# Performance work log

Measured on AMD Instinct MI355X. Metric: run time of the kernel, lower is better.

Reference implementation:

```python
import jax, jax.numpy as jnp
import numpy as np
from jax import lax

GROUPS = 4
KH = KW = 3
K = KH * KW
STRIDE = (1, 1)
PAD = ((1, 1), (1, 1))
DIL = (1, 1)


def _bilinear_gather(padded, py, px):
    # padded: (B,C,Hp,Wp); py,px: (B,C,K,Ho,Wo) float sample positions in padded coords
    B, C, Hp, Wp = padded.shape
    bi = jnp.arange(B)[:, None, None, None, None]
    ci = jnp.arange(C)[None, :, None, None, None]
    y0 = jnp.floor(py)
    x0 = jnp.floor(px)
    wy = py - y0
    wx = px - x0
    out = jnp.zeros(py.shape, padded.dtype)
    corners = ((0, 0, (1 - wy) * (1 - wx)), (0, 1, (1 - wy) * wx),
               (1, 0, wy * (1 - wx)), (1, 1, wy * wx))
    for dy, dx, w in corners:
        yy = y0 + dy
        xx = x0 + dx
        valid = (yy >= 0) & (yy < Hp) & (xx >= 0) & (xx < Wp)  # zero outside (implicit zero padding)
        yc = jnp.clip(yy, 0, Hp - 1).astype(jnp.int32)
        xc = jnp.clip(xx, 0, Wp - 1).astype(jnp.int32)
        out = out + jnp.where(valid, padded[bi, ci, yc, xc] * w, 0.0)
    return out


def deform_conv2d(inps, weight, bias, weight_off, bias_off):
    B, C, H, W = inps.shape
    # offset/mask predicting conv (grouped, same geometry as the main conv)
    off = lax.conv_general_dilated(inps, weight_off, STRIDE, PAD, rhs_dilation=DIL,
                                   feature_group_count=GROUPS,
                                   dimension_numbers=('NCHW', 'OIHW', 'NCHW'))
    off = off + bias_off[None, :, None, None]
    Ho, Wo = off.shape[2], off.shape[3]
    off = off.reshape(B, 3, C * K, Ho, Wo)  # (B, dim+1, C*K, Ho, Wo)
    dy = off[:, 0].reshape(B, C, K, Ho, Wo)
    dx = off[:, 1].reshape(B, C, K, Ho, Wo)
    # softmax across the GROUP axis, as in the original reshape(b,1,groups,-1,h,w).softmax(dim=2)
    mask = jax.nn.softmax(off[:, 2].reshape(B, GROUPS, (C // GROUPS) * K, Ho, Wo), axis=1)
    mask = mask.reshape(B, C, K, Ho, Wo)

    padded = jnp.pad(inps, ((0, 0), (0, 0), PAD[0], PAD[1]))
    ky, kx = jnp.meshgrid(jnp.arange(KH), jnp.arange(KW), indexing='ij')
    ky = ky.ravel().astype(inps.dtype)
    kx = kx.ravel().astype(inps.dtype)
    oh = jnp.arange(Ho, dtype=inps.dtype)
    ow = jnp.arange(Wo, dtype=inps.dtype)
    # sample position per (batch, in-channel, kernel tap, output pixel)
    py = oh[None, None, None, :, None] * STRIDE[0] + ky[None, None, :, None, None] * DIL[0] + dy
    px = ow[None, None, None, None, :] * STRIDE[1] + kx[None, None, :, None, None] * DIL[1] + dx

    sampled = _bilinear_gather(padded, py, px) * mask  # (B,C,K,Ho,Wo)

    Cout = weight.shape[0]
    Cg = C // GROUPS
    wg = weight.reshape(GROUPS, Cout // GROUPS, Cg, K)          # (g, o, c, k)
    sg = sampled.reshape(B, GROUPS, Cg, K, Ho, Wo)              # (b, g, c, k, h, w)
    out = jnp.einsum('bgckhw,gock->bgohw', sg, wg).reshape(B, Cout, Ho, Wo)
    return out + bias[None, :, None, None]


def setup_inputs() -> dict:
    key = jax.random.key(0)
    k0, k1, k2, k3 = jax.random.split(key, 4)
    B, C, H, W = 8, 64, 64, 64
    Cout = 64
    inps = jax.random.normal(k0, (B, C, H, W), dtype=jnp.float32)
    weight = jax.random.normal(k1, (Cout, C // GROUPS, KH, KW), dtype=jnp.float32) * 0.05
    bias = jax.random.normal(k2, (Cout,), dtype=jnp.float32) * 0.05
    # small offset-conv weights -> offsets of a few pixels, non-saturated softmax
    weight_off = jax.random.normal(k3, (C * K * 3, C // GROUPS, KH, KW), dtype=jnp.float32) * 0.05
    bias_off = jnp.zeros((C * K * 3,), dtype=jnp.float32)
    return {'inps': inps, 'weight': weight, 'bias': bias,
            'weight_off': weight_off, 'bias_off': bias_off}


def reference(inps, weight, bias, weight_off, bias_off):
    return deform_conv2d(inps, weight, bias, weight_off, bias_off)
```

## Files before the change

kernel.cpp:

```cpp
#include <hip/hip_runtime.h>

typedef __attribute__((ext_vector_type(8))) short short8;
typedef __attribute__((ext_vector_type(4))) float f32x4;

__device__ __forceinline__ unsigned short bf16rne(float f) {
    unsigned u = __float_as_uint(f);
    u += 0x7FFFu + ((u >> 16) & 1u);
    return (unsigned short)(u >> 16);
}
__device__ __forceinline__ float bf16dec(unsigned short h) {
    return __uint_as_float((unsigned)h << 16);
}
__device__ __forceinline__ unsigned cvtpk2(float lo, float hi) {
    unsigned r;
    asm("v_cvt_pk_bf16_f32 %0, %1, %2" : "=v"(r) : "v"(lo), "v"(hi));
    return r;
}

extern __shared__ char smem[];


#define IMC4_OFF   0
#define PATCH4_OFF 37376
#define SX4_OFF    62720
#define LGX4_OFF   72960
#define LDS_V4     77312
#define OTB4_OFF   37376

#define PWOFF_U32  138240
#define PWM_U32    5120
#define WS_NEEDED  ((size_t)(PWOFF_U32 + PWM_U32) * 4)

__global__ __launch_bounds__(256)
void pack_weights(const float* __restrict__ wmain,
                  const float* __restrict__ woff,
                  unsigned* __restrict__ pw)
{
    int idx = blockIdx.x * 256 + threadIdx.x;
    if (idx < PWOFF_U32) {
        int j2   = idx & 3;
        int lane = (idx >> 2) & 63;
        int rest = idx >> 8;
        int kt   = rest % 5;
        int t    = rest / 5;
        int comp = t / 36, r36 = t - comp * 36;
        int jw   = r36 / 9, ntg = r36 - jw * 9;
        int ochb = comp * 576 + jw * 144 + ntg * 16;
        int g    = ochb / 432;
        int ktf  = (9 * g) >> 1;
        int och  = ochb + (lane & 15);
        int ck   = (ktf + kt) * 32 + (lane >> 4) * 8 + j2 * 2 - g * 144;
        float v0 = 0.f, v1 = 0.f;
        if ((unsigned)ck < 144u)       v0 = woff[(size_t)och * 144 + ck];
        if ((unsigned)(ck + 1) < 144u) v1 = woff[(size_t)och * 144 + ck + 1];
        pw[idx] = (unsigned)bf16rne(v0) | ((unsigned)bf16rne(v1) << 16);
    } else if (idx < PWOFF_U32 + PWM_U32) {
        int m    = idx - PWOFF_U32;
        int j2   = m & 3;
        int lane = (m >> 2) & 63;
        int rest = m >> 8;
        int jw   = rest / 5, pair = rest - jw * 5;
        int och  = jw * 16 + (lane & 15);
        int w0   = pair * 32 + (lane >> 4) * 8 + j2 * 2;
        float v0 = (w0 < 144)     ? wmain[(size_t)och * 144 + w0]     : 0.f;
        float v1 = (w0 + 1 < 144) ? wmain[(size_t)och * 144 + w0 + 1] : 0.f;
        pw[idx] = (unsigned)bf16rne(v0) | ((unsigned)bf16rne(v1) << 16);
    }
}

__global__ __launch_bounds__(256, 2)
void deform_v4(const float* __restrict__ inps,
               const float* __restrict__ bmain,
               const float* __restrict__ boff,
               const unsigned short* __restrict__ pwoff,
               const unsigned short* __restrict__ pwm,
               float* __restrict__ out)
{
    unsigned short* IMC   = (unsigned short*)(smem + IMC4_OFF);
    unsigned short* PATCH = (unsigned short*)(smem + PATCH4_OFF);
    unsigned short* SX    = (unsigned short*)(smem + SX4_OFF);
    unsigned short* LGX   = (unsigned short*)(smem + LGX4_OFF);
    float*          OTB   = (float*)(smem + OTB4_OFF);

    const int tid  = threadIdx.x;
    const int lane = tid & 63;
    const int jw   = __builtin_amdgcn_readfirstlane(tid >> 6);
    const int slot = lane & 15;
    const int q    = lane >> 4;

    const int b    = blockIdx.x >> 7;
    const int tile = blockIdx.x & 127;
    const int ty0  = (tile >> 3) << 2;
    const int tx0  = (tile & 7) << 3;

    const float* inb = inps + (size_t)b * 262144;

    for (int e = tid; e < 12288; e += 256) {
        int c = e / 192, rem = e - c * 192;
        int y = rem >> 4, x = rem & 15;
        int gy = ty0 + y - 4, gx = tx0 + x - 4;
        float v = 0.f;
        if ((unsigned)gy < 64u && (unsigned)gx < 64u)
            v = inb[(c * 64 + gy) * 64 + gx];
        PATCH[c * 198 + rem] = bf16rne(v);
    }
    __syncthreads();

    {
        const int px  = tid >> 3;
        const int sub = tid & 7;
        const int pyr = px >> 3, pxx = px & 7;
        unsigned* dst = (unsigned*)(IMC + px * 584);
        #pragma unroll 4
        for (int i = 0; i < 36; ++i) {
            int kk = i * 16 + sub * 2;
            int c0 = kk / 9,        r0 = kk - c0 * 9;
            int c1 = (kk + 1) / 9,  r1 = (kk + 1) - c1 * 9;
            unsigned short a  = PATCH[c0 * 198 + (pyr + r0 / 3 + 3) * 16 + pxx + r0 % 3 + 3];
            unsigned short bb = PATCH[c1 * 198 + (pyr + r1 / 3 + 3) * 16 + pxx + r1 % 3 + 3];
            dst[(unsigned)kk >> 1] = (unsigned)a | ((unsigned)bb << 16);
        }
    }
    __syncthreads();

    f32x4 aco[2] = {{0.f,0.f,0.f,0.f},{0.f,0.f,0.f,0.f}};

    auto pair_mfma = [&](int pair) {
        const short8 bfr = ((const short8*)pwm)[(jw * 5 + pair) * 64 + lane];
        #pragma unroll
        for (int mt = 0; mt < 2; ++mt) {
            const short8 a8 = *(const short8*)(SX + jw * 1280 + (mt * 16 + slot) * 40 + q * 8);
            aco[mt] = __builtin_amdgcn_mfma_f32_16x16x32_bf16(a8, bfr, aco[mt], 0, 0, 0);
        }
    };

    for (int ntg = 0; ntg < 9; ++ntg) {
        f32x4 aD[2] = {{0.f,0.f,0.f,0.f},{0.f,0.f,0.f,0.f}};
        f32x4 aX[2] = {{0.f,0.f,0.f,0.f},{0.f,0.f,0.f,0.f}};
        f32x4 aM[2] = {{0.f,0.f,0.f,0.f},{0.f,0.f,0.f,0.f}};

        auto gemm3 = [&](f32x4* acc, int comp) {
            const int ochb = comp * 576 + jw * 144 + ntg * 16;
            const int g    = ochb / 432;
            const int ktf  = (9 * g) >> 1;
            const int t    = comp * 36 + jw * 9 + ntg;
            const short8* wp  = (const short8*)pwoff + t * 320 + lane;
            const short8* ap0 = (const short8*)(smem + IMC4_OFF);
            #pragma unroll
            for (int kt = 0; kt < 5; ++kt) {
                const short8 bfr = wp[kt * 64];
                const int ktg = ktf + kt;
                #pragma unroll
                for (int mt = 0; mt < 2; ++mt) {
                    const short8 af = ap0[(mt * 16 + slot) * 73 + ktg * 4 + q];
                    acc[mt] = __builtin_amdgcn_mfma_f32_16x16x32_bf16(af, bfr, acc[mt], 0, 0, 0);
                }
            }
            const float bo = boff[ochb + slot];
            #pragma unroll
            for (int mt = 0; mt < 2; ++mt) {
                acc[mt][0] += bo; acc[mt][1] += bo; acc[mt][2] += bo; acc[mt][3] += bo;
            }
        };
        gemm3(aD, 0); gemm3(aX, 1); gemm3(aM, 2);

        #pragma unroll
        for (int mt = 0; mt < 2; ++mt)
        #pragma unroll
        for (int r = 0; r < 4; ++r) {
            int pxr = mt * 16 + q * 4 + r;
            LGX[pxr * 68 + slot * 4 + jw] = bf16rne(aM[mt][r]);
        }
        __syncthreads();

        const int rr  = ntg * 16 + slot;
        const int cg  = rr / 9;
        const int kk9 = rr - cg * 9;
        const int kyk = kk9 / 3, kxk = kk9 - kyk * 3;
        const int c   = jw * 16 + cg;
        const float* inc = inb + c * 4096;
        const int pbase = c * 198;
        const int par = ntg & 1;

        #pragma unroll
        for (int mt = 0; mt < 2; ++mt)
        #pragma unroll
        for (int r = 0; r < 4; ++r) {
            const int pxr = mt * 16 + q * 4 + r;
            const int pyr = pxr >> 3, pxx = pxr & 7;
            const float own = aM[mt][r];

            const uint2 lg = *(const uint2*)(LGX + pxr * 68 + slot * 4);
            float s4 = __expf(bf16dec((unsigned short)(lg.x & 0xFFFF)) - own)
                     + __expf(bf16dec((unsigned short)(lg.x >> 16))    - own)
                     + __expf(bf16dec((unsigned short)(lg.y & 0xFFFF)) - own)
                     + __expf(bf16dec((unsigned short)(lg.y >> 16))    - own);
            const float msk = 1.0f / s4;

            float pyf = (float)(ty0 + pyr + kyk - 1) + aD[mt][r];
            float pxf = (float)(tx0 + pxx + kxk - 1) + aX[mt][r];
            float y0f = floorf(pyf), x0f = floorf(pxf);
            float wy = pyf - y0f, wx = pxf - x0f;
            int iy0 = (int)y0f, ix0 = (int)x0f;
            float w00 = (1.f - wy) * (1.f - wx), w01 = (1.f - wy) * wx;
            float w10 = wy * (1.f - wx),         w11 = wy * wx;

            int ly0 = iy0 - ty0 + 4;
            int lx0 = ix0 - tx0 + 4;
            float v;
            if ((unsigned)ly0 < 11u && (unsigned)lx0 < 15u) {
                const int a = pbase + ly0 * 16 + lx0;
                v = w00 * bf16dec(PATCH[a])      + w01 * bf16dec(PATCH[a + 1])
                  + w10 * bf16dec(PATCH[a + 16]) + w11 * bf16dec(PATCH[a + 17]);
            } else {
                v = 0.f;
                if ((unsigned)iy0 < 64u) {
                    if ((unsigned)ix0 < 64u)       v += w00 * inc[iy0 * 64 + ix0];
                    if ((unsigned)(ix0 + 1) < 64u) v += w01 * inc[iy0 * 64 + ix0 + 1];
                }
                if ((unsigned)(iy0 + 1) < 64u) {
                    if ((unsigned)ix0 < 64u)       v += w10 * inc[(iy0 + 1) * 64 + ix0];
                    if ((unsigned)(ix0 + 1) < 64u) v += w11 * inc[(iy0 + 1) * 64 + ix0 + 1];
                }
            }
            SX[jw * 1280 + pxr * 40 + par * 16 + slot] = bf16rne(v * msk);
        }

        if (ntg & 1)  { asm volatile("" ::: "memory"); pair_mfma(ntg >> 1); }
        if (ntg == 8) { asm volatile("" ::: "memory"); pair_mfma(4); }
        __syncthreads();
    }

    {
        const int o = jw * 16 + slot;
        const float bo = bmain[o];
        #pragma unroll
        for (int mt = 0; mt < 2; ++mt)
        #pragma unroll
        for (int r = 0; r < 4; ++r)
            OTB[o * 33 + mt * 16 + q * 4 + r] = aco[mt][r] + bo;
    }
    __syncthreads();
    #pragma unroll
    for (int i = 0; i < 8; ++i) {
        int f  = i * 256 + tid;
        int oo = f >> 5, pp = f & 31;
        out[(size_t)(b * 64 + oo) * 4096 + (ty0 + (pp >> 3)) * 64 + (tx0 + (pp & 7))] =
            OTB[oo * 33 + pp];
    }
}

#define V2IMC_OFF   0
#define V2S_OFF     37376
#define V2LGX_OFF   74752
#define V2LDS_BYTES 78848

__global__ __launch_bounds__(256, 2)
void deform_v2(const float* __restrict__ inps,
               const float* __restrict__ wmain,
               const float* __restrict__ bmain,
               const float* __restrict__ woff,
               const float* __restrict__ boff,
               float* __restrict__ out)
{
    unsigned short* IMC  = (unsigned short*)(smem + V2IMC_OFF);
    unsigned short* SBUF = (unsigned short*)(smem + V2S_OFF);
    unsigned short* LGX  = (unsigned short*)(smem + V2LGX_OFF);
    float* PATCH = (float*)(smem + V2S_OFF);
    float* OTB   = (float*)(smem + V2IMC_OFF);

    const int tid  = threadIdx.x;
    const int lane = tid & 63;
    const int jw   = __builtin_amdgcn_readfirstlane(tid >> 6);
    const int slot = lane & 15;
    const int q    = lane >> 4;

    const int b    = blockIdx.x >> 7;
    const int tile = blockIdx.x & 127;
    const int ty0  = (tile >> 3) << 2;
    const int tx0  = (tile & 7) << 3;

    const float* inb = inps + (size_t)b * 262144;

    for (int e = tid; e < 64 * 60; e += 256) {
        int ch = e / 60, rem = e - ch * 60;
        int iy = rem / 10, ix = rem - iy * 10;
        int gy = ty0 + iy - 1, gx = tx0 + ix - 1;
        float v = 0.f;
        if ((unsigned)gy < 64u && (unsigned)gx < 64u)
            v = inb[(ch * 64 + gy) * 64 + gx];
        PATCH[ch * 61 + rem] = v;
    }
    __syncthreads();
    {
        const int px  = tid >> 3;
        const int sub = tid & 7;
        const int pyr = px >> 3, pxx = px & 7;
        unsigned short* dst = IMC + px * 584;
        for (int i = 0; i < 36; ++i) {
            int kk = sub * 72 + 2 * i;
            float v0, v1;
            { int c = kk / 9, r9 = kk - c * 9, ky = r9 / 3, kx = r9 - ky * 3;
              v0 = PATCH[c * 61 + (pyr + ky) * 10 + (pxx + kx)]; }
            { int k1 = kk + 1; int c = k1 / 9, r9 = k1 - c * 9, ky = r9 / 3, kx = r9 - ky * 3;
              v1 = PATCH[c * 61 + (pyr + ky) * 10 + (pxx + kx)]; }
            *(unsigned*)(dst + kk) = cvtpk2(v0, v1);
        }
    }
    __syncthreads();

    for (int ntg = 0; ntg < 9; ++ntg) {
        f32x4 aD[2] = {{0.f,0.f,0.f,0.f},{0.f,0.f,0.f,0.f}};
        f32x4 aX[2] = {{0.f,0.f,0.f,0.f},{0.f,0.f,0.f,0.f}};
        f32x4 aM[2] = {{0.f,0.f,0.f,0.f},{0.f,0.f,0.f,0.f}};

        auto gemm3 = [&](f32x4* acc, int comp) {
            const int ochb = comp * 576 + jw * 144 + ntg * 16;
            const int g    = ochb / 432;
            const int ktf  = (9 * g) >> 1;
            const int ch0  = g * 18;
            const int och  = ochb + slot;
            #pragma unroll
            for (int kt = 0; kt < 5; ++kt) {
                const int ktg   = ktf + kt;
                const int chunk = ktg * 4 + q;
                short8 bfr;
                if ((unsigned)(chunk - ch0) < 18u) {
                    const float4* wp = (const float4*)(woff + (size_t)och * 144 + (chunk - ch0) * 8);
                    float4 w0 = wp[0], w1 = wp[1];
                    union { unsigned u[4]; short8 s; } cv;
                    cv.u[0] = cvtpk2(w0.x, w0.y); cv.u[1] = cvtpk2(w0.z, w0.w);
                    cv.u[2] = cvtpk2(w1.x, w1.y); cv.u[3] = cvtpk2(w1.z, w1.w);
                    bfr = cv.s;
                } else {
                    bfr = short8{0,0,0,0,0,0,0,0};
                }
                #pragma unroll
                for (int mt = 0; mt < 2; ++mt) {
                    const short8* ap = (const short8*)(smem + V2IMC_OFF +
                                        (mt * 16 + slot) * 1168 + ktg * 64 + q * 16);
                    acc[mt] = __builtin_amdgcn_mfma_f32_16x16x32_bf16(*ap, bfr, acc[mt], 0, 0, 0);
                }
            }
            const float bo = boff[ochb + slot];
            #pragma unroll
            for (int mt = 0; mt < 2; ++mt) {
                acc[mt][0] += bo; acc[mt][1] += bo; acc[mt][2] += bo; acc[mt][3] += bo;
            }
        };
        gemm3(aD, 0); gemm3(aX, 1); gemm3(aM, 2);

        #pragma unroll
        for (int mt = 0; mt < 2; ++mt)
        #pragma unroll
        for (int r = 0; r < 4; ++r) {
            int pxr = mt * 16 + q * 4 + r;
            LGX[(jw * 32 + pxr) * 16 + slot] = bf16rne(aM[mt][r]);
        }
        __syncthreads();

        const int rr  = ntg * 16 + slot;
        const int cg  = rr / 9;
        const int kk9 = rr - cg * 9;
        const int kyk = kk9 / 3, kxk = kk9 - kyk * 3;
        const float* inc = inb + (jw * 16 + cg) * 4096;

        #pragma unroll
        for (int mt = 0; mt < 2; ++mt)
        #pragma unroll
        for (int r = 0; r < 4; ++r) {
            const int pxr = mt * 16 + q * 4 + r;
            const int pyr = pxr >> 3, pxx = pxr & 7;
            float own = aM[mt][r];
            float l0 = (jw == 0) ? own : bf16dec(LGX[(0 * 32 + pxr) * 16 + slot]);
            float l1 = (jw == 1) ? own : bf16dec(LGX[(1 * 32 + pxr) * 16 + slot]);
            float l2 = (jw == 2) ? own : bf16dec(LGX[(2 * 32 + pxr) * 16 + slot]);
            float l3 = (jw == 3) ? own : bf16dec(LGX[(3 * 32 + pxr) * 16 + slot]);
            float m4 = fmaxf(fmaxf(l0, l1), fmaxf(l2, l3));
            float s4 = __expf(l0 - m4) + __expf(l1 - m4) + __expf(l2 - m4) + __expf(l3 - m4);
            float msk = __expf(own - m4) / s4;

            float pyf = (float)(ty0 + pyr + kyk - 1) + aD[mt][r];
            float pxf = (float)(tx0 + pxx + kxk - 1) + aX[mt][r];
            float y0f = floorf(pyf), x0f = floorf(pxf);
            float wy = pyf - y0f, wx = pxf - x0f;
            int iy0 = (int)y0f, ix0 = (int)x0f;
            float w00 = (1.f - wy) * (1.f - wx), w01 = (1.f - wy) * wx;
            float w10 = wy * (1.f - wx),         w11 = wy * wx;
            float v = 0.f;
            if ((unsigned)iy0 < 64u) {
                if ((unsigned)ix0 < 64u)       v += w00 * inc[iy0 * 64 + ix0];
                if ((unsigned)(ix0 + 1) < 64u) v += w01 * inc[iy0 * 64 + ix0 + 1];
            }
            if ((unsigned)(iy0 + 1) < 64u) {
                if ((unsigned)ix0 < 64u)       v += w10 * inc[(iy0 + 1) * 64 + ix0];
                if ((unsigned)(ix0 + 1) < 64u) v += w11 * inc[(iy0 + 1) * 64 + ix0 + 1];
            }
            SBUF[pxr * 584 + jw * 144 + rr] = bf16rne(v * msk);
        }
        __syncthreads();
    }

    {
        f32x4 aco2[2] = {{0.f,0.f,0.f,0.f},{0.f,0.f,0.f,0.f}};
        const int ktf = (9 * jw) >> 1;
        const int ch0 = jw * 18;
        const int o   = jw * 16 + slot;
        #pragma unroll
        for (int kt = 0; kt < 5; ++kt) {
            const int ktg   = ktf + kt;
            const int chunk = ktg * 4 + q;
            short8 bfr;
            if ((unsigned)(chunk - ch0) < 18u) {
                const float4* wp = (const float4*)(wmain + (size_t)o * 144 + (chunk - ch0) * 8);
                float4 w0 = wp[0], w1 = wp[1];
                union { unsigned u[4]; short8 s; } cv;
                cv.u[0] = cvtpk2(w0.x, w0.y); cv.u[1] = cvtpk2(w0.z, w0.w);
                cv.u[2] = cvtpk2(w1.x, w1.y); cv.u[3] = cvtpk2(w1.z, w1.w);
                bfr = cv.s;
            } else {
                bfr = short8{0,0,0,0,0,0,0,0};
            }
            #pragma unroll
            for (int mt = 0; mt < 2; ++mt) {
                const short8* ap = (const short8*)(smem + V2S_OFF +
                                    (mt * 16 + slot) * 1168 + ktg * 64 + q * 16);
                aco2[mt] = __builtin_amdgcn_mfma_f32_16x16x32_bf16(*ap, bfr, aco2[mt], 0, 0, 0);
            }
        }
        const float bo = bmain[o];
        __syncthreads();
        #pragma unroll
        for (int mt = 0; mt < 2; ++mt)
        #pragma unroll
        for (int r = 0; r < 4; ++r)
            OTB[o * 33 + mt * 16 + q * 4 + r] = aco2[mt][r] + bo;
    }
    __syncthreads();
    #pragma unroll
    for (int i = 0; i < 8; ++i) {
        int f  = i * 256 + tid;
        int oo = f >> 5, pp = f & 31;
        out[(size_t)(b * 64 + oo) * 4096 + (ty0 + (pp >> 3)) * 64 + (tx0 + (pp & 7))] =
            OTB[oo * 33 + pp];
    }
}

extern "C" void kernel_launch(void* const* d_in, const int* in_sizes, int n_in,
                              void* d_out, int out_size, void* d_ws, size_t ws_size,
                              hipStream_t stream) {
    const float* inps   = (const float*)d_in[0];
    const float* weight = (const float*)d_in[1];
    const float* bias   = (const float*)d_in[2];
    const float* woff   = (const float*)d_in[3];
    const float* boff   = (const float*)d_in[4];
    float* outp = (float*)d_out;

    if (ws_size >= WS_NEEDED) {
        unsigned* pw = (unsigned*)d_ws;
        pack_weights<<<dim3(560), dim3(256), 0, stream>>>(weight, woff, pw);
        hipFuncSetAttribute((const void*)deform_v4,
                            hipFuncAttributeMaxDynamicSharedMemorySize, LDS_V4);
        deform_v4<<<dim3(1024), dim3(256), LDS_V4, stream>>>(
            inps, bias, boff,
            (const unsigned short*)pw,
            (const unsigned short*)(pw + PWOFF_U32), outp);
    } else {
        hipFuncSetAttribute((const void*)deform_v2,
                            hipFuncAttributeMaxDynamicSharedMemorySize, V2LDS_BYTES);
        deform_v2<<<dim3(1024), dim3(256), V2LDS_BYTES, stream>>>(
            inps, weight, bias, woff, boff, outp);
    }
}
```

Before: 141.9 us.

## Drop explicit im2col buffer; read offset-conv A operands from channel-minor patch

Removes the explicit im2col staging pass and its large LDS buffer. The input patch is now stored channel-minor (pixel-major, padded stride 66), so the offset-conv MFMA A fragments are read straight from the patch. The offset weights are repacked so K runs tap-major with channels contiguous. This frees LDS, letting launch bounds rise from 2 to 4 blocks per CU for more occupancy, at the cost of scattered, possibly bank-conflicting patch reads during bilinear sampling and changed SX/LGX strides.

```diff
diff --git a/kernel.cpp b/kernel.cpp
--- a/kernel.cpp
+++ b/kernel.cpp
@@ -20,12 +20,11 @@
 extern __shared__ char smem[];
 
 
-#define IMC4_OFF   0
-#define PATCH4_OFF 37376
-#define SX4_OFF    62720
-#define LGX4_OFF   72960
-#define LDS_V4     77312
-#define OTB4_OFF   37376
+#define PT5_OFF   0
+#define SX5_OFF   25344
+#define LGX5_OFF  34560
+#define LDS_V5    38656
+#define OTB5_OFF  0
 
 #define PWOFF_U32  138240
 #define PWM_U32    5120
@@ -49,10 +48,13 @@
         int g    = ochb / 432;
         int ktf  = (9 * g) >> 1;
         int och  = ochb + (lane & 15);
-        int ck   = (ktf + kt) * 32 + (lane >> 4) * 8 + j2 * 2 - g * 144;
+        int w    = (ktf + kt) * 32 + (lane >> 4) * 8 + j2 * 2 - g * 144;
         float v0 = 0.f, v1 = 0.f;
-        if ((unsigned)ck < 144u)       v0 = woff[(size_t)och * 144 + ck];
-        if ((unsigned)(ck + 1) < 144u) v1 = woff[(size_t)och * 144 + ck + 1];
+        if ((unsigned)w < 144u)
+            v0 = woff[(size_t)och * 144 + (w & 15) * 9 + (w >> 4)];
+        int w1 = w + 1;
+        if ((unsigned)w1 < 144u)
+            v1 = woff[(size_t)och * 144 + (w1 & 15) * 9 + (w1 >> 4)];
         pw[idx] = (unsigned)bf16rne(v0) | ((unsigned)bf16rne(v1) << 16);
     } else if (idx < PWOFF_U32 + PWM_U32) {
         int m    = idx - PWOFF_U32;
@@ -68,25 +70,26 @@
     }
 }
 
-__global__ __launch_bounds__(256, 2)
-void deform_v4(const float* __restrict__ inps,
+__global__ __launch_bounds__(256, 4)
+void deform_v5(const float* __restrict__ inps,
                const float* __restrict__ bmain,
                const float* __restrict__ boff,
                const unsigned short* __restrict__ pwoff,
                const unsigned short* __restrict__ pwm,
                float* __restrict__ out)
 {
-    unsigned short* IMC   = (unsigned short*)(smem + IMC4_OFF);
-    unsigned short* PATCH = (unsigned short*)(smem + PATCH4_OFF);
-    unsigned short* SX    = (unsigned short*)(smem + SX4_OFF);
-    unsigned short* LGX   = (unsigned short*)(smem + LGX4_OFF);
-    float*          OTB   = (float*)(smem + OTB4_OFF);
+    unsigned short* PT  = (unsigned short*)(smem + PT5_OFF);
+    unsigned short* SX  = (unsigned short*)(smem + SX5_OFF);
+    unsigned short* LGX = (unsigned short*)(smem + LGX5_OFF);
+    float*          OTB = (float*)(smem + OTB5_OFF);
 
     const int tid  = threadIdx.x;
     const int lane = tid & 63;
     const int jw   = __builtin_amdgcn_readfirstlane(tid >> 6);
     const int slot = lane & 15;
     const int q    = lane >> 4;
+    const int pyr0 = slot >> 3;
+    const int pxx0 = slot & 7;
 
     const int b    = blockIdx.x >> 7;
     const int tile = blockIdx.x & 127;
@@ -96,30 +99,15 @@
     const float* inb = inps + (size_t)b * 262144;
 
     for (int e = tid; e < 12288; e += 256) {
-        int c = e / 192, rem = e - c * 192;
+        int c = e >> 6;
+        c = e / 192;
+        int rem = e - c * 192;
         int y = rem >> 4, x = rem & 15;
         int gy = ty0 + y - 4, gx = tx0 + x - 4;
         float v = 0.f;
         if ((unsigned)gy < 64u && (unsigned)gx < 64u)
             v = inb[(c * 64 + gy) * 64 + gx];
-        PATCH[c * 198 + rem] = bf16rne(v);
-    }
-    __syncthreads();
-
-    {
-        const int px  = tid >> 3;
-        const int sub = tid & 7;
-        const int pyr = px >> 3, pxx = px & 7;
-        unsigned* dst = (unsigned*)(IMC + px * 584);
-        #pragma unroll 4
-        for (int i = 0; i < 36; ++i) {
-            int kk = i * 16 + sub * 2;
-            int c0 = kk / 9,        r0 = kk - c0 * 9;
-            int c1 = (kk + 1) / 9,  r1 = (kk + 1) - c1 * 9;
-            unsigned short a  = PATCH[c0 * 198 + (pyr + r0 / 3 + 3) * 16 + pxx + r0 % 3 + 3];
-            unsigned short bb = PATCH[c1 * 198 + (pyr + r1 / 3 + 3) * 16 + pxx + r1 % 3 + 3];
-            dst[(unsigned)kk >> 1] = (unsigned)a | ((unsigned)bb << 16);
-        }
+        PT[rem * 66 + c] = bf16rne(v);
     }
     __syncthreads();
 
@@ -129,7 +117,7 @@
         const short8 bfr = ((const short8*)pwm)[(jw * 5 + pair) * 64 + lane];
         #pragma unroll
         for (int mt = 0; mt < 2; ++mt) {
-            const short8 a8 = *(const short8*)(SX + jw * 1280 + (mt * 16 + slot) * 40 + q * 8);
+            const short8 a8 = *(const short8*)(SX + jw * 1152 + (mt * 16 + slot) * 36 + q * 8);
             aco[mt] = __builtin_amdgcn_mfma_f32_16x16x32_bf16(a8, bfr, aco[mt], 0, 0, 0);
         }
     };
@@ -140,21 +128,27 @@
         f32x4 aM[2] = {{0.f,0.f,0.f,0.f},{0.f,0.f,0.f,0.f}};
 
         auto gemm3 = [&](f32x4* acc, int comp) {
-            const int ochb = comp * 576 + jw * 144 + ntg * 16;
-            const int g    = ochb / 432;
-            const int ktf  = (9 * g) >> 1;
-            const int t    = comp * 36 + jw * 9 + ntg;
-            const short8* wp  = (const short8*)pwoff + t * 320 + lane;
-            const short8* ap0 = (const short8*)(smem + IMC4_OFF);
+            const int ochb   = comp * 576 + jw * 144 + ntg * 16;
+            const int g      = ochb / 432;
+            const int ktf    = (9 * g) >> 1;
+            const int t      = comp * 36 + jw * 9 + ntg;
+            const short8* wp = (const short8*)pwoff + t * 320 + lane;
+            const int w8base = ktf * 32 + q * 8 - g * 144;
+            const int gc16   = g * 16;
             #pragma unroll
             for (int kt = 0; kt < 5; ++kt) {
                 const short8 bfr = wp[kt * 64];
-                const int ktg = ktf + kt;
-                #pragma unroll
-                for (int mt = 0; mt < 2; ++mt) {
-                    const short8 af = ap0[(mt * 16 + slot) * 73 + ktg * 4 + q];
-                    acc[mt] = __builtin_amdgcn_mfma_f32_16x16x32_bf16(af, bfr, acc[mt], 0, 0, 0);
-                }
+                int wc = w8base + kt * 32;
+                wc = wc < 0 ? 0 : (wc > 136 ? 136 : wc);
+                const int tap = wc >> 4;
+                const int ky  = (tap * 11) >> 5;
+                const int kx  = tap - ky * 3;
+                const int a0  = ((pyr0 + ky + 3) * 16 + (pxx0 + kx + 3)) * 66
+                                + gc16 + (wc & 15);
+                const short8 af0 = *(const short8*)(PT + a0);
+                const short8 af1 = *(const short8*)(PT + a0 + 2112);
+                acc[0] = __builtin_amdgcn_mfma_f32_16x16x32_bf16(af0, bfr, acc[0], 0, 0, 0);
+                acc[1] = __builtin_amdgcn_mfma_f32_16x16x32_bf16(af1, bfr, acc[1], 0, 0, 0);
             }
             const float bo = boff[ochb + slot];
             #pragma unroll
@@ -169,7 +163,7 @@
         #pragma unroll
         for (int r = 0; r < 4; ++r) {
             int pxr = mt * 16 + q * 4 + r;
-            LGX[pxr * 68 + slot * 4 + jw] = bf16rne(aM[mt][r]);
+            LGX[pxr * 64 + slot * 4 + jw] = bf16rne(aM[mt][r]);
         }
         __syncthreads();
 
@@ -179,7 +173,6 @@
         const int kyk = kk9 / 3, kxk = kk9 - kyk * 3;
         const int c   = jw * 16 + cg;
         const float* inc = inb + c * 4096;
-        const int pbase = c * 198;
         const int par = ntg & 1;
 
         #pragma unroll
@@ -190,7 +183,7 @@
             const int pyr = pxr >> 3, pxx = pxr & 7;
             const float own = aM[mt][r];
 
-            const uint2 lg = *(const uint2*)(LGX + pxr * 68 + slot * 4);
+            const uint2 lg = *(const uint2*)(LGX + pxr * 64 + slot * 4);
             float s4 = __expf(bf16dec((unsigned short)(lg.x & 0xFFFF)) - own)
                      + __expf(bf16dec((unsigned short)(lg.x >> 16))    - own)
                      + __expf(bf16dec((unsigned short)(lg.y & 0xFFFF)) - own)
@@ -209,9 +202,9 @@
             int lx0 = ix0 - tx0 + 4;
             float v;
             if ((unsigned)ly0 < 11u && (unsigned)lx0 < 15u) {
-                const int a = pbase + ly0 * 16 + lx0;
-                v = w00 * bf16dec(PATCH[a])      + w01 * bf16dec(PATCH[a + 1])
-                  + w10 * bf16dec(PATCH[a + 16]) + w11 * bf16dec(PATCH[a + 17]);
+                const int a = (ly0 * 16 + lx0) * 66 + c;
+                v = w00 * bf16dec(PT[a])        + w01 * bf16dec(PT[a + 66])
+                  + w10 * bf16dec(PT[a + 1056]) + w11 * bf16dec(PT[a + 1122]);
             } else {
                 v = 0.f;
                 if ((unsigned)iy0 < 64u) {
@@ -223,7 +216,7 @@
                     if ((unsigned)(ix0 + 1) < 64u) v += w11 * inc[(iy0 + 1) * 64 + ix0 + 1];
                 }
             }
-            SX[jw * 1280 + pxr * 40 + par * 16 + slot] = bf16rne(v * msk);
+            SX[jw * 1152 + pxr * 36 + par * 16 + slot] = bf16rne(v * msk);
         }
 
         if (ntg & 1)  { asm volatile("" ::: "memory"); pair_mfma(ntg >> 1); }
@@ -459,9 +452,9 @@
     if (ws_size >= WS_NEEDED) {
         unsigned* pw = (unsigned*)d_ws;
         pack_weights<<<dim3(560), dim3(256), 0, stream>>>(weight, woff, pw);
-        hipFuncSetAttribute((const void*)deform_v4,
-                            hipFuncAttributeMaxDynamicSharedMemorySize, LDS_V4);
-        deform_v4<<<dim3(1024), dim3(256), LDS_V4, stream>>>(
+        hipFuncSetAttribute((const void*)deform_v5,
+                            hipFuncAttributeMaxDynamicSharedMemorySize, LDS_V5);
+        deform_v5<<<dim3(1024), dim3(256), LDS_V5, stream>>>(
             inps, bias, boff,
             (const unsigned short*)pw,
             (const unsigned short*)(pw + PWOFF_U32), outp);
```

New measurement: 176.9 us. +24.6%, slower.
